# Performance work log

Hardware: AMD Instinct MI355X
Metric: run time of the kernel (lower is better)

## Reference

```python
import jax, jax.numpy as jnp
import numpy as np

B, S, M, D, H = 2, 2048, 512, 1024, 16
HD = D // H      # head dim 64
KVC = D // 16    # MLA kv compression dim 64
QC = D // 32     # MLA q compression dim 32
RD = HD          # retrieval (qk) head dim 64
LOOKBACK = 8     # cross_window
EPS = 1e-6


def rmsnorm(x, w):
    return x * jax.lax.rsqrt(jnp.mean(x * x, axis=-1, keepdims=True) + EPS) * w


def setup_inputs():
    key = jax.random.key(0)
    ks = jax.random.split(key, 20)
    g = lambda i, shape: jax.random.normal(ks[i], shape, jnp.float32) * 0.02
    return {
        "x": jax.random.normal(ks[0], (B, S, D), jnp.float32),
        "memory": jax.random.normal(ks[1], (B, M, D), jnp.float32),
        "seg_ids": jnp.sort(jax.random.randint(ks[2], (B, S), 0, M), axis=-1),
        "norm1_w": jnp.ones((D,), jnp.float32),
        "W_dq": g(3, (D, QC)),
        "W_uq": g(4, (QC, H * RD)),
        "W_dkv": g(5, (D, KVC)),
        "W_uk": g(6, (KVC, H * RD)),
        "W_uv": g(7, (KVC, H * HD)),
        "W_o_self": g(8, (H * HD, D)),
        "norm2_w": jnp.ones((D,), jnp.float32),
        "W_q_c": g(9, (D, D)),
        "W_k_c": g(10, (D, D)),
        "W_v_c": g(11, (D, D)),
        "W_o_c": g(12, (D, D)),
        "norm3_w": jnp.ones((D,), jnp.float32),
        "W_gate": g(13, (D, 4 * D)),
        "W_up": g(14, (D, 4 * D)),
        "W_down": g(15, (4 * D, D)),
    }


def reference(x, memory, seg_ids, norm1_w, W_dq, W_uq, W_dkv, W_uk, W_uv,
              W_o_self, norm2_w, W_q_c, W_k_c, W_v_c, W_o_c, norm3_w,
              W_gate, W_up, W_down):
    # ---- MLA causal self-attention (low-rank compressed q/kv) ----
    h = rmsnorm(x, norm1_w)
    q = ((h @ W_dq) @ W_uq).reshape(B, S, H, RD)
    c_kv = h @ W_dkv                                  # [B,S,KVC]
    k = (c_kv @ W_uk).reshape(B, S, H, RD)
    v = (c_kv @ W_uv).reshape(B, S, H, HD)
    scores = jnp.einsum('bihd,bjhd->bhij', q, k) / np.float32(np.sqrt(RD))
    causal = jnp.tril(jnp.ones((S, S), bool))
    scores = jnp.where(causal, scores, -jnp.inf)
    attn = jax.nn.softmax(scores, axis=-1)
    o = jnp.einsum('bhij,bjhd->bihd', attn, v).reshape(B, S, H * HD)
    x = x + o @ W_o_self
    # ---- segment sliding-window cross-attention ----
    h = rmsnorm(x, norm2_w)
    qc = (h @ W_q_c).reshape(B, S, H, HD)
    kc = (memory @ W_k_c).reshape(B, M, H, HD)
    vc = (memory @ W_v_c).reshape(B, M, H, HD)
    sc = jnp.einsum('bihd,bjhd->bhij', qc, kc) / np.float32(np.sqrt(HD))
    kv_pos = jnp.arange(M)
    seg = seg_ids[:, :, None]                          # [B,S,1]
    allowed = (kv_pos[None, None, :] <= seg) & (kv_pos[None, None, :] >= seg - LOOKBACK)
    sc = jnp.where(allowed[:, None, :, :], sc, -jnp.inf)
    ac = jax.nn.softmax(sc, axis=-1)
    oc = jnp.einsum('bhij,bjhd->bihd', ac, vc).reshape(B, S, D)
    x = x + oc @ W_o_c
    # ---- SwiGLU FFN ----
    h = rmsnorm(x, norm3_w)
    x = x + (jax.nn.silu(h @ W_gate) * (h @ W_up)) @ W_down
    return x
```

## Files before the change

### kernel.cpp

```cpp
#include <hip/hip_runtime.h>
#include <stdint.h>

typedef unsigned short U16;
typedef __bf16 bf16x8 __attribute__((ext_vector_type(8)));
typedef unsigned short us8 __attribute__((ext_vector_type(8)));
typedef float f32x4 __attribute__((ext_vector_type(4)));

__device__ __forceinline__ U16 f2bf(float f) {
    unsigned u = __builtin_bit_cast(unsigned, f);
    unsigned r = (u + 0x7fff + ((u >> 16) & 1)) >> 16;
    return (U16)r;
}
__device__ __forceinline__ float bf2f(U16 v) {
    return __builtin_bit_cast(float, (unsigned)v << 16);
}
__device__ __forceinline__ bf16x8 ld8(const U16* p) { return __builtin_bit_cast(bf16x8, *(const us8*)p); }

__device__ __forceinline__ void async16(const U16* g, U16* l) {
    auto* gp = (const __attribute__((address_space(1))) U16*)g;
    auto* lp = (__attribute__((address_space(3))) U16*)(uintptr_t)(uint32_t)(uintptr_t)l;
    __builtin_amdgcn_global_load_lds(gp, lp, 16, 0, 0);
}

struct WEnt { const float* src; U16* dst; int K, N, Kpad, Npad, koff, noff, tiles; };
struct WTable { WEnt e[13]; };

__global__ __launch_bounds__(256) void wtrans_all(WTable t) {
    int bx = blockIdx.x, ei = 0;
    while (bx >= t.e[ei].tiles) { bx -= t.e[ei].tiles; ei++; }
    const WEnt E = t.e[ei];
    const int ntn = E.Npad >> 5;
    const int n0 = (bx % ntn) * 32, k0 = (bx / ntn) * 32;
    __shared__ float tile[32][33];
    const int tx = threadIdx.x & 31, ty = threadIdx.x >> 5;
#pragma unroll
    for (int i = 0; i < 4; i++) {
        int kk = k0 + ty + i * 8, n = n0 + tx;
        int k = kk - E.koff;
        float v = (k >= 0 && k < E.K && n < E.N) ? E.src[(size_t)k * E.N + n] : 0.f;
        tile[ty + i * 8][tx] = v;
    }
    __syncthreads();
#pragma unroll
    for (int i = 0; i < 4; i++) {
        int n = n0 + ty + i * 8, kk = k0 + tx;
        E.dst[(size_t)(E.noff + n) * E.Kpad + kk] = f2bf(tile[tx][ty + i * 8]);
    }
}

__global__ __launch_bounds__(256) void f2bf_k(const float* __restrict__ in, U16* __restrict__ out, int n) {
    int i = (blockIdx.x * 256 + threadIdx.x) * 4;
    if (i < n) {
        float4 v = *(const float4*)(in + i);
        out[i + 0] = f2bf(v.x); out[i + 1] = f2bf(v.y);
        out[i + 2] = f2bf(v.z); out[i + 3] = f2bf(v.w);
    }
}

__global__ __launch_bounds__(256) void rmsnorm_k(const float* __restrict__ x, const float* __restrict__ w,
                                                 U16* __restrict__ h) {
    const int row = blockIdx.x, tid = threadIdx.x;
    const float4 v = *(const float4*)(x + (size_t)row * 1024 + tid * 4);
    float ss = v.x * v.x + v.y * v.y + v.z * v.z + v.w * v.w;
#pragma unroll
    for (int o = 32; o > 0; o >>= 1) ss += __shfl_xor(ss, o);
    __shared__ float red[4];
    if ((tid & 63) == 0) red[tid >> 6] = ss;
    __syncthreads();
    float tot = red[0] + red[1] + red[2] + red[3];
    float sc = rsqrtf(tot * (1.0f / 1024.0f) + 1e-6f);
    const float4 wv = *(const float4*)(w + tid * 4);
    U16* hp = h + (size_t)row * 1024 + tid * 4;
    hp[0] = f2bf(v.x * sc * wv.x); hp[1] = f2bf(v.y * sc * wv.y);
    hp[2] = f2bf(v.z * sc * wv.z); hp[3] = f2bf(v.w * sc * wv.w);
}

template <int EPI>
__global__ __launch_bounds__(256) void gemm2(const U16* __restrict__ A, const U16* __restrict__ Bt,
                                             void* __restrict__ Cout, const float* __restrict__ resid,
                                             int M, int N, int K, int lda, int ldc) {
    __shared__ __align__(16) U16 As[2][128 * 32];
    __shared__ __align__(16) U16 Bs[2][128 * 32];
    const int tid = threadIdx.x;
    const int m0 = blockIdx.y * 128, n0 = blockIdx.x * 128;
    const int wave = tid >> 6, lane = tid & 63, l16 = lane & 15, quad = lane >> 4;
    const int wm = (wave >> 1) * 64, wn = (wave & 1) * 64;
    const int sr = lane >> 2, sc = (lane & 3) * 8;
    const U16* gA = A + (size_t)(m0 + wave * 32 + sr) * lda + sc;
    const U16* gB = Bt + (size_t)(n0 + wave * 32 + sr) * K + sc;
    f32x4 acc[4][4] = {};
    for (int kt = 0; kt < K; kt += 64) {
        __syncthreads();
#pragma unroll
        for (int p = 0; p < 2; p++) {
            const int o = kt + p * 32;
            async16(gA + o, &As[p][(wave * 32) * 32]);
            async16(gA + (size_t)16 * lda + o, &As[p][(wave * 32 + 16) * 32]);
            async16(gB + o, &Bs[p][(wave * 32) * 32]);
            async16(gB + (size_t)16 * K + o, &Bs[p][(wave * 32 + 16) * 32]);
        }
        __syncthreads();
#pragma unroll
        for (int p = 0; p < 2; p++) {
            bf16x8 af[4], bfr[4];
#pragma unroll
            for (int i = 0; i < 4; i++) {
                af[i]  = ld8(&As[p][(wm + i * 16 + l16) * 32 + quad * 8]);
                bfr[i] = ld8(&Bs[p][(wn + i * 16 + l16) * 32 + quad * 8]);
            }
#pragma unroll
            for (int mi = 0; mi < 4; mi++)
#pragma unroll
                for (int ni = 0; ni < 4; ni++)
                    acc[mi][ni] = __builtin_amdgcn_mfma_f32_16x16x32_bf16(af[mi], bfr[ni], acc[mi][ni], 0, 0, 0);
        }
    }
#pragma unroll
    for (int mi = 0; mi < 4; mi++) {
#pragma unroll
        for (int r = 0; r < 4; r++) {
            int m = m0 + wm + mi * 16 + quad * 4 + r;
#pragma unroll
            for (int ni = 0; ni < 4; ni++) {
                int n = n0 + wn + ni * 16 + l16;
                float val = acc[mi][ni][r];
                if (EPI == 0) ((U16*)Cout)[(size_t)m * ldc + n] = f2bf(val);
                else if (EPI == 1) ((float*)Cout)[(size_t)m * ldc + n] = resid[(size_t)m * ldc + n] + val;
                else ((U16*)Cout)[(size_t)n * ldc + m] = f2bf(val);
            }
        }
    }
}

template <int EPI>
__global__ __launch_bounds__(256) void gemm_m64(const U16* __restrict__ A, const U16* __restrict__ Bt,
                                                void* __restrict__ Cout, const float* __restrict__ resid,
                                                int M, int N, int K, int lda, int ldb, int ldc) {
    __shared__ __align__(16) U16 As[4][64 * 32];
    __shared__ __align__(16) U16 Bs[4][128 * 32];
    const int tid = threadIdx.x;
    const int m0 = blockIdx.y * 64, n0 = blockIdx.x * 128;
    const int k0 = blockIdx.z * K;
    const int wave = tid >> 6, lane = tid & 63, l16 = lane & 15, quad = lane >> 4;
    const int wm = (wave >> 1) * 32, wn = (wave & 1) * 64;
    const int sr = lane >> 2, sc = (lane & 3) * 8;
    const U16* gA = A + (size_t)(m0 + wave * 16 + sr) * lda + sc + k0;
    const U16* gB = Bt + (size_t)(n0 + wave * 32 + sr) * ldb + sc + k0;
    f32x4 acc[2][4] = {};
    for (int kt = 0; kt < K; kt += 128) {
        __syncthreads();
#pragma unroll
        for (int p = 0; p < 4; p++) {
            const int o = kt + p * 32;
            async16(gA + o, &As[p][(wave * 16) * 32]);
            async16(gB + o, &Bs[p][(wave * 32) * 32]);
            async16(gB + (size_t)16 * ldb + o, &Bs[p][(wave * 32 + 16) * 32]);
        }
        __syncthreads();
#pragma unroll
        for (int p = 0; p < 4; p++) {
            bf16x8 af[2], bfr[4];
#pragma unroll
            for (int i = 0; i < 2; i++)
                af[i] = ld8(&As[p][(wm + i * 16 + l16) * 32 + quad * 8]);
#pragma unroll
            for (int i = 0; i < 4; i++)
                bfr[i] = ld8(&Bs[p][(wn + i * 16 + l16) * 32 + quad * 8]);
#pragma unroll
            for (int mi = 0; mi < 2; mi++)
#pragma unroll
                for (int ni = 0; ni < 4; ni++)
                    acc[mi][ni] = __builtin_amdgcn_mfma_f32_16x16x32_bf16(af[mi], bfr[ni], acc[mi][ni], 0, 0, 0);
        }
    }
#pragma unroll
    for (int mi = 0; mi < 2; mi++) {
#pragma unroll
        for (int r = 0; r < 4; r++) {
            int m = m0 + wm + mi * 16 + quad * 4 + r;
#pragma unroll
            for (int ni = 0; ni < 4; ni++) {
                int n = n0 + wn + ni * 16 + l16;
                float val = acc[mi][ni][r];
                if (EPI == 0) ((U16*)Cout)[(size_t)m * ldc + n] = f2bf(val);
                else if (EPI == 1) ((float*)Cout)[(size_t)m * ldc + n] = resid[(size_t)m * ldc + n] + val;
                else if (EPI == 3) atomicAdd(&((float*)Cout)[(size_t)m * ldc + n], val);
            }
        }
    }
}

__global__ __launch_bounds__(256) void ffn1_fused(const U16* __restrict__ A, const U16* __restrict__ Wgu,
                                                  U16* __restrict__ Cout) {
    __shared__ __align__(16) U16 As[2][128 * 32];
    __shared__ __align__(16) U16 Gs[2][64 * 32];
    __shared__ __align__(16) U16 Us[2][64 * 32];
    const int tid = threadIdx.x;
    const int m0 = blockIdx.y * 128, n0 = blockIdx.x * 64;
    const int wave = tid >> 6, lane = tid & 63, l16 = lane & 15, quad = lane >> 4;
    const int wm = (wave >> 1) * 64, wn = (wave & 1) * 32;
    const int sr = lane >> 2, sc = (lane & 3) * 8;
    const U16* gA = A + (size_t)(m0 + wave * 32 + sr) * 1024 + sc;
    const U16* gG = Wgu + (size_t)(n0 + wave * 16 + sr) * 1024 + sc;
    const U16* gU = gG + (size_t)4096 * 1024;
    f32x4 ag[4][2] = {}, au[4][2] = {};
    for (int kt = 0; kt < 1024; kt += 64) {
        __syncthreads();
#pragma unroll
        for (int p = 0; p < 2; p++) {
            const int o = kt + p * 32;
            async16(gA + o, &As[p][(wave * 32) * 32]);
            async16(gA + 16 * 1024 + o, &As[p][(wave * 32 + 16) * 32]);
            async16(gG + o, &Gs[p][(wave * 16) * 32]);
            async16(gU + o, &Us[p][(wave * 16) * 32]);
        }
        __syncthreads();
#pragma unroll
        for (int p = 0; p < 2; p++) {
            bf16x8 af[4], bg[2], bu[2];
#pragma unroll
            for (int i = 0; i < 4; i++)
                af[i] = ld8(&As[p][(wm + i * 16 + l16) * 32 + quad * 8]);
#pragma unroll
            for (int i = 0; i < 2; i++) {
                bg[i] = ld8(&Gs[p][(wn + i * 16 + l16) * 32 + quad * 8]);
                bu[i] = ld8(&Us[p][(wn + i * 16 + l16) * 32 + quad * 8]);
            }
#pragma unroll
            for (int mi = 0; mi < 4; mi++)
#pragma unroll
                for (int ni = 0; ni < 2; ni++) {
                    ag[mi][ni] = __builtin_amdgcn_mfma_f32_16x16x32_bf16(af[mi], bg[ni], ag[mi][ni], 0, 0, 0);
                    au[mi][ni] = __builtin_amdgcn_mfma_f32_16x16x32_bf16(af[mi], bu[ni], au[mi][ni], 0, 0, 0);
                }
        }
    }
#pragma unroll
    for (int mi = 0; mi < 4; mi++) {
#pragma unroll
        for (int r = 0; r < 4; r++) {
            int m = m0 + wm + mi * 16 + quad * 4 + r;
#pragma unroll
            for (int ni = 0; ni < 2; ni++) {
                int n = n0 + wn + ni * 16 + l16;
                float g = ag[mi][ni][r], u = au[mi][ni][r];
                float act = g / (1.f + __expf(-g)) * u;
                Cout[(size_t)m * 4096 + n] = f2bf(act);
            }
        }
    }
}

__global__ __launch_bounds__(256) void flash_self3(const U16* __restrict__ QK, const U16* __restrict__ Vt,
                                                   U16* __restrict__ Og) {
    __shared__ __align__(16) U16 Ps[4 * 1280];
    __shared__ float Ored[4 * 2080];
    __shared__ float Lred[128];
    const int wave = threadIdx.x >> 6, lane = threadIdx.x & 63;
    const int l16 = lane & 15, quad = lane >> 4;
    const int bx = blockIdx.x;
    const int t = 63 - (bx >> 5);
    const int bh = bx & 31, b = bh >> 4, h = bh & 15;
    const int q0 = t * 32;
    const size_t rowQ0 = (size_t)(b * 2048 + q0 + l16) * 2048 + h * 64;
    const size_t rowQ1 = rowQ0 + 16 * 2048;
    bf16x8 aq[2][2];
    aq[0][0] = ld8(QK + rowQ0 + quad * 8);  aq[0][1] = ld8(QK + rowQ0 + 32 + quad * 8);
    aq[1][0] = ld8(QK + rowQ1 + quad * 8);  aq[1][1] = ld8(QK + rowQ1 + 32 + quad * 8);
    const U16* Kbase = QK + (size_t)(b * 2048) * 2048 + 1024 + h * 64;
    const U16* Vbase = Vt + (size_t)(h * 64) * 4096 + b * 2048;
    f32x4 o[2][4] = {};
    float ls[2][4] = {};
    U16* Pw = &Ps[wave * 1280];
    const int prd = l16 * 40 + ((quad ^ (l16 >> 2)) << 3);
    const int jend = q0 + 32;
    for (int j0 = wave * 32; j0 < jend; j0 += 128) {
        const U16* kp = Kbase + (size_t)j0 * 2048;
        bf16x8 b00 = ld8(kp + (size_t)l16 * 2048 + quad * 8);
        bf16x8 b01 = ld8(kp + (size_t)l16 * 2048 + 32 + quad * 8);
        bf16x8 b10 = ld8(kp + (size_t)(16 + l16) * 2048 + quad * 8);
        bf16x8 b11 = ld8(kp + (size_t)(16 + l16) * 2048 + 32 + quad * 8);
        bf16x8 v0 = ld8(Vbase + (size_t)(0  + l16) * 4096 + j0 + quad * 8);
        bf16x8 v1 = ld8(Vbase + (size_t)(16 + l16) * 4096 + j0 + quad * 8);
        bf16x8 v2 = ld8(Vbase + (size_t)(32 + l16) * 4096 + j0 + quad * 8);
        bf16x8 v3 = ld8(Vbase + (size_t)(48 + l16) * 4096 + j0 + quad * 8);
        f32x4 s[2][2] = {};
#pragma unroll
        for (int g = 0; g < 2; g++) {
            s[g][0] = __builtin_amdgcn_mfma_f32_16x16x32_bf16(aq[g][0], b00, s[g][0], 0, 0, 0);
            s[g][0] = __builtin_amdgcn_mfma_f32_16x16x32_bf16(aq[g][1], b01, s[g][0], 0, 0, 0);
            s[g][1] = __builtin_amdgcn_mfma_f32_16x16x32_bf16(aq[g][0], b10, s[g][1], 0, 0, 0);
            s[g][1] = __builtin_amdgcn_mfma_f32_16x16x32_bf16(aq[g][1], b11, s[g][1], 0, 0, 0);
        }
        float p0[2][4], p1[2][4];
        if (j0 + 32 >= jend) {
#pragma unroll
            for (int g = 0; g < 2; g++)
#pragma unroll
                for (int r = 0; r < 4; r++) {
                    int qg = q0 + g * 16 + quad * 4 + r;
                    p0[g][r] = (j0 + l16 <= qg) ? __expf(fminf(s[g][0][r] * 0.125f, 30.f)) : 0.f;
                    p1[g][r] = (j0 + 16 + l16 <= qg) ? __expf(fminf(s[g][1][r] * 0.125f, 30.f)) : 0.f;
                }
        } else {
#pragma unroll
            for (int g = 0; g < 2; g++)
#pragma unroll
                for (int r = 0; r < 4; r++) {
                    p0[g][r] = __expf(fminf(s[g][0][r] * 0.125f, 30.f));
                    p1[g][r] = __expf(fminf(s[g][1][r] * 0.125f, 30.f));
                }
        }
#pragma unroll
        for (int g = 0; g < 2; g++)
#pragma unroll
            for (int r = 0; r < 4; r++) {
                ls[g][r] += p0[g][r] + p1[g][r];
                int row = quad * 4 + r;
                Pw[g * 640 + row * 40 + ((((l16 >> 3) + 0) ^ quad) << 3) + (l16 & 7)] = f2bf(p0[g][r]);
                Pw[g * 640 + row * 40 + ((((l16 >> 3) + 2) ^ quad) << 3) + (l16 & 7)] = f2bf(p1[g][r]);
            }
#pragma unroll
        for (int g = 0; g < 2; g++) {
            bf16x8 ap = ld8(&Pw[g * 640 + prd]);
            o[g][0] = __builtin_amdgcn_mfma_f32_16x16x32_bf16(ap, v0, o[g][0], 0, 0, 0);
            o[g][1] = __builtin_amdgcn_mfma_f32_16x16x32_bf16(ap, v1, o[g][1], 0, 0, 0);
            o[g][2] = __builtin_amdgcn_mfma_f32_16x16x32_bf16(ap, v2, o[g][2], 0, 0, 0);
            o[g][3] = __builtin_amdgcn_mfma_f32_16x16x32_bf16(ap, v3, o[g][3], 0, 0, 0);
        }
    }
    float* Or = &Ored[wave * 2080];
#pragma unroll
    for (int g = 0; g < 2; g++) {
#pragma unroll
        for (int dg = 0; dg < 4; dg++)
#pragma unroll
            for (int r = 0; r < 4; r++)
                Or[(g * 16 + quad * 4 + r) * 65 + dg * 16 + l16] = o[g][dg][r];
#pragma unroll
        for (int r = 0; r < 4; r++) {
            float v = ls[g][r];
            v += __shfl_xor(v, 1); v += __shfl_xor(v, 2);
            v += __shfl_xor(v, 4); v += __shfl_xor(v, 8);
            if (l16 == 0) Lred[wave * 32 + g * 16 + quad * 4 + r] = v;
        }
    }
    __syncthreads();
    const int q = threadIdx.x >> 3, d0 = (threadIdx.x & 7) * 8;
    float l = Lred[q] + Lred[32 + q] + Lred[64 + q] + Lred[96 + q];
    float inv = 1.0f / l;
    us8 outv;
#pragma unroll
    for (int i = 0; i < 8; i++) {
        int idx = q * 65 + d0 + i;
        float s = Ored[idx] + Ored[2080 + idx] + Ored[4160 + idx] + Ored[6240 + idx];
        outv[i] = f2bf(s * inv);
    }
    *(us8*)(Og + (size_t)(b * 2048 + q0 + q) * 1024 + h * 64 + d0) = outv;
}

__global__ __launch_bounds__(256) void cross_attn(const U16* __restrict__ qc, const U16* __restrict__ kvc,
                                                  const int* __restrict__ seg_ids, U16* __restrict__ oc) {
    const int tok = blockIdx.x;
    const int b = tok >> 11;
    const int w = threadIdx.x >> 6, lane = threadIdx.x & 63;
    const int h = blockIdx.y * 4 + w;
    const int seg = seg_ids[tok];
    const size_t qoff = (size_t)tok * 1024 + h * 64 + lane;
    float q = bf2f(qc[qoff]);
    float s[9];
#pragma unroll
    for (int jj = 0; jj < 9; jj++) {
        int j = seg - 8 + jj;
        float sc = -INFINITY;
        if (j >= 0) {
            float kv = bf2f(kvc[((size_t)(b * 512) + j) * 2048 + h * 64 + lane]);
            sc = q * kv;
            sc += __shfl_xor(sc, 1); sc += __shfl_xor(sc, 2); sc += __shfl_xor(sc, 4);
            sc += __shfl_xor(sc, 8); sc += __shfl_xor(sc, 16); sc += __shfl_xor(sc, 32);
            sc *= 0.125f;
        }
        s[jj] = sc;
    }
    float m = s[0];
#pragma unroll
    for (int jj = 1; jj < 9; jj++) m = fmaxf(m, s[jj]);
    float l = 0.f, o = 0.f;
#pragma unroll
    for (int jj = 0; jj < 9; jj++) {
        int j = seg - 8 + jj;
        if (j >= 0) {
            float p = __expf(s[jj] - m);
            l += p;
            o += p * bf2f(kvc[((size_t)(b * 512) + j) * 2048 + 1024 + h * 64 + lane]);
        }
    }
    oc[qoff] = f2bf(o / l);
}

extern "C" void kernel_launch(void* const* d_in, const int* in_sizes, int n_in,
                              void* d_out, int out_size, void* d_ws, size_t ws_size,
                              hipStream_t stream) {
    const float* x      = (const float*)d_in[0];
    const float* memory = (const float*)d_in[1];
    const int*   seg    = (const int*)d_in[2];
    const float* n1w    = (const float*)d_in[3];
    const float* W_dq   = (const float*)d_in[4];
    const float* W_uq   = (const float*)d_in[5];
    const float* W_dkv  = (const float*)d_in[6];
    const float* W_uk   = (const float*)d_in[7];
    const float* W_uv   = (const float*)d_in[8];
    const float* W_os   = (const float*)d_in[9];
    const float* n2w    = (const float*)d_in[10];
    const float* W_qc   = (const float*)d_in[11];
    const float* W_kc   = (const float*)d_in[12];
    const float* W_vc   = (const float*)d_in[13];
    const float* W_oc   = (const float*)d_in[14];
    const float* n3w    = (const float*)d_in[15];
    const float* W_gate = (const float*)d_in[16];
    const float* W_up   = (const float*)d_in[17];
    const float* W_down = (const float*)d_in[18];
    (void)in_sizes; (void)n_in; (void)out_size; (void)ws_size;

    char* ws = (char*)d_ws;
    size_t off = 0;
    auto alloc = [&](size_t bytes) -> void* {
        void* p = ws + off;
        off += (bytes + 255) & ~(size_t)255;
        return p;
    };
    const size_t MB = 1024 * 1024;
    U16* hbuf     = (U16*)alloc(8 * MB);
    float* x1     = (float*)alloc(16 * MB);
    float* x2     = (float*)alloc(16 * MB);
    float* cq32   = (float*)alloc(2 * MB);
    U16* Wt_dqkv  = (U16*)alloc(128 * 1024 * 2);
    U16* Wt_uqk   = (U16*)alloc(2048 * 128 * 2);
    U16* Wt_uv    = (U16*)alloc(1024 * 128 * 2);
    U16* Wt_os    = (U16*)alloc(1024 * 1024 * 2);
    U16* Wt_qc    = (U16*)alloc(1024 * 1024 * 2);
    U16* Wt_kvc   = (U16*)alloc((size_t)2048 * 1024 * 2);
    U16* Wt_oc    = (U16*)alloc(1024 * 1024 * 2);
    U16* Wt_gu    = (U16*)alloc((size_t)8192 * 1024 * 2);
    U16* Wt_down  = (U16*)alloc((size_t)1024 * 4096 * 2);
    U16* mem_bf   = (U16*)alloc(1024 * 1024 * 2);
    char* arena   = ws + off;
    U16* cq  = (U16*)(arena);
    U16* qkb = (U16*)(arena + 1 * MB);
    U16* vt  = (U16*)(arena + 17 * MB);
    U16* ob  = (U16*)(arena + 25 * MB);
    U16* qcb  = (U16*)(arena);
    U16* kvcb = (U16*)(arena + 8 * MB);
    U16* ocb  = (U16*)(arena + 12 * MB);
    U16* gact = (U16*)(arena);

    WTable T;
    int i = 0;
    auto ent = [&](const float* s, U16* d, int K, int N, int Kpad, int Npad, int koff, int noff) {
        T.e[i++] = WEnt{s, d, K, N, Kpad, Npad, koff, noff, (Kpad >> 5) * (Npad >> 5)};
    };
    ent(W_dq,   Wt_dqkv, 1024, 32,   1024, 32,   0,  0);
    ent(W_dkv,  Wt_dqkv, 1024, 64,   1024, 96,   0,  32);
    ent(W_uq,   Wt_uqk,  32,   1024, 128,  1024, 0,  0);
    ent(W_uk,   Wt_uqk,  64,   1024, 128,  1024, 32, 1024);
    ent(W_uv,   Wt_uv,   64,   1024, 128,  1024, 32, 0);
    ent(W_os,   Wt_os,   1024, 1024, 1024, 1024, 0,  0);
    ent(W_qc,   Wt_qc,   1024, 1024, 1024, 1024, 0,  0);
    ent(W_kc,   Wt_kvc,  1024, 1024, 1024, 1024, 0,  0);
    ent(W_vc,   Wt_kvc,  1024, 1024, 1024, 1024, 0,  1024);
    ent(W_oc,   Wt_oc,   1024, 1024, 1024, 1024, 0,  0);
    ent(W_gate, Wt_gu,   1024, 4096, 1024, 4096, 0,  0);
    ent(W_up,   Wt_gu,   1024, 4096, 1024, 4096, 0,  4096);
    ent(W_down, Wt_down, 4096, 1024, 4096, 1024, 0,  0);
    int total_tiles = 0;
    for (int j = 0; j < 13; j++) total_tiles += T.e[j].tiles;
    wtrans_all<<<total_tiles, 256, 0, stream>>>(T);
    f2bf_k<<<1024, 256, 0, stream>>>(memory, mem_bf, 1024 * 1024);
    hipMemsetAsync(cq32, 0, (size_t)4096 * 128 * 4, stream);

    rmsnorm_k<<<4096, 256, 0, stream>>>(x, n1w, hbuf);
    gemm_m64<3><<<dim3(1, 64, 4), 256, 0, stream>>>(hbuf, Wt_dqkv, cq32, nullptr, 4096, 128, 256, 1024, 1024, 128);
    f2bf_k<<<512, 256, 0, stream>>>(cq32, cq, 4096 * 128);
    gemm2<0><<<dim3(16, 32), 256, 0, stream>>>(cq, Wt_uqk, qkb, nullptr, 4096, 2048, 128, 128, 2048);
    gemm2<2><<<dim3(8, 32),  256, 0, stream>>>(cq, Wt_uv,  vt,  nullptr, 4096, 1024, 128, 128, 4096);
    flash_self3<<<2048, 256, 0, stream>>>(qkb, vt, ob);
    gemm_m64<1><<<dim3(8, 64), 256, 0, stream>>>(ob, Wt_os, x1, x, 4096, 1024, 1024, 1024, 1024, 1024);

    rmsnorm_k<<<4096, 256, 0, stream>>>(x1, n2w, hbuf);
    gemm_m64<0><<<dim3(8, 64),  256, 0, stream>>>(hbuf,   Wt_qc,  qcb,  nullptr, 4096, 1024, 1024, 1024, 1024, 1024);
    gemm_m64<0><<<dim3(16, 16), 256, 0, stream>>>(mem_bf, Wt_kvc, kvcb, nullptr, 1024, 2048, 1024, 1024, 1024, 2048);
    cross_attn<<<dim3(4096, 4), 256, 0, stream>>>(qcb, kvcb, seg, ocb);
    gemm_m64<1><<<dim3(8, 64),  256, 0, stream>>>(ocb,    Wt_oc,  x2,   x1,      4096, 1024, 1024, 1024, 1024, 1024);

    rmsnorm_k<<<4096, 256, 0, stream>>>(x2, n3w, hbuf);
    ffn1_fused<<<dim3(64, 32), 256, 0, stream>>>(hbuf, Wt_gu, gact);
    gemm_m64<1><<<dim3(8, 64), 256, 0, stream>>>(gact, Wt_down, (float*)d_out, x2, 4096, 1024, 4096, 4096, 4096, 1024);
}
```

Baseline: 553.5 us.

## Split-K down-projection with atomic adds, LDS-staged transpose epilogue, faster bf16 rounding

The FFN down-projection now runs on the 128x128 gemm2 tile with the K=4096 reduction split in two along grid z. Each half atomically adds into a zero-initialised output, and the first half also adds the residual. The transposed-V epilogue of gemm2 now stages results through LDS and writes 16-byte coalesced rows instead of scattered 2-byte stores. The softmax P conversion also uses a cheaper round-half-up bf16 conversion. These add an output memset, a second LDS buffer and fp32 atomics, which make the output summation order nondeterministic.

```diff
diff --git a/kernel.cpp b/kernel.cpp
--- a/kernel.cpp
+++ b/kernel.cpp
@@ -10,6 +10,9 @@
     unsigned u = __builtin_bit_cast(unsigned, f);
     unsigned r = (u + 0x7fff + ((u >> 16) & 1)) >> 16;
     return (U16)r;
+}
+__device__ __forceinline__ U16 f2bf_fast(float f) {
+    return (U16)((__builtin_bit_cast(unsigned, f) + 0x8000u) >> 16);
 }
 __device__ __forceinline__ float bf2f(U16 v) {
     return __builtin_bit_cast(float, (unsigned)v << 16);
@@ -78,16 +81,17 @@
 template <int EPI>
 __global__ __launch_bounds__(256) void gemm2(const U16* __restrict__ A, const U16* __restrict__ Bt,
                                              void* __restrict__ Cout, const float* __restrict__ resid,
-                                             int M, int N, int K, int lda, int ldc) {
+                                             int M, int N, int K, int lda, int ldb, int ldc) {
     __shared__ __align__(16) U16 As[2][128 * 32];
     __shared__ __align__(16) U16 Bs[2][128 * 32];
     const int tid = threadIdx.x;
     const int m0 = blockIdx.y * 128, n0 = blockIdx.x * 128;
+    const int k0 = blockIdx.z * K;
     const int wave = tid >> 6, lane = tid & 63, l16 = lane & 15, quad = lane >> 4;
     const int wm = (wave >> 1) * 64, wn = (wave & 1) * 64;
     const int sr = lane >> 2, sc = (lane & 3) * 8;
-    const U16* gA = A + (size_t)(m0 + wave * 32 + sr) * lda + sc;
-    const U16* gB = Bt + (size_t)(n0 + wave * 32 + sr) * K + sc;
+    const U16* gA = A + (size_t)(m0 + wave * 32 + sr) * lda + sc + k0;
+    const U16* gB = Bt + (size_t)(n0 + wave * 32 + sr) * ldb + sc + k0;
     f32x4 acc[4][4] = {};
     for (int kt = 0; kt < K; kt += 64) {
         __syncthreads();
@@ -97,7 +101,7 @@
             async16(gA + o, &As[p][(wave * 32) * 32]);
             async16(gA + (size_t)16 * lda + o, &As[p][(wave * 32 + 16) * 32]);
             async16(gB + o, &Bs[p][(wave * 32) * 32]);
-            async16(gB + (size_t)16 * K + o, &Bs[p][(wave * 32 + 16) * 32]);
+            async16(gB + (size_t)16 * ldb + o, &Bs[p][(wave * 32 + 16) * 32]);
         }
         __syncthreads();
 #pragma unroll
@@ -115,18 +119,38 @@
                     acc[mi][ni] = __builtin_amdgcn_mfma_f32_16x16x32_bf16(af[mi], bfr[ni], acc[mi][ni], 0, 0, 0);
         }
     }
-#pragma unroll
-    for (int mi = 0; mi < 4; mi++) {
-#pragma unroll
-        for (int r = 0; r < 4; r++) {
-            int m = m0 + wm + mi * 16 + quad * 4 + r;
-#pragma unroll
-            for (int ni = 0; ni < 4; ni++) {
-                int n = n0 + wn + ni * 16 + l16;
-                float val = acc[mi][ni][r];
-                if (EPI == 0) ((U16*)Cout)[(size_t)m * ldc + n] = f2bf(val);
-                else if (EPI == 1) ((float*)Cout)[(size_t)m * ldc + n] = resid[(size_t)m * ldc + n] + val;
-                else ((U16*)Cout)[(size_t)n * ldc + m] = f2bf(val);
+    if constexpr (EPI == 2) {
+        __shared__ __align__(16) U16 Ts[4][64 * 80];
+        U16* T = Ts[wave];
+#pragma unroll
+        for (int mi = 0; mi < 4; mi++)
+#pragma unroll
+            for (int ni = 0; ni < 4; ni++)
+#pragma unroll
+                for (int r = 0; r < 4; r++)
+                    T[(ni * 16 + l16) * 80 + mi * 16 + quad * 4 + r] = f2bf(acc[mi][ni][r]);
+#pragma unroll
+        for (int c = 0; c < 8; c++) {
+            int nloc = (lane >> 3) + 8 * c, mloc = (lane & 7) * 8;
+            us8 v = *(const us8*)&T[nloc * 80 + mloc];
+            *(us8*)&((U16*)Cout)[(size_t)(n0 + wn + nloc) * ldc + (m0 + wm + mloc)] = v;
+        }
+    } else {
+#pragma unroll
+        for (int mi = 0; mi < 4; mi++) {
+#pragma unroll
+            for (int r = 0; r < 4; r++) {
+                int m = m0 + wm + mi * 16 + quad * 4 + r;
+#pragma unroll
+                for (int ni = 0; ni < 4; ni++) {
+                    int n = n0 + wn + ni * 16 + l16;
+                    float val = acc[mi][ni][r];
+                    if (EPI == 0) ((U16*)Cout)[(size_t)m * ldc + n] = f2bf(val);
+                    else if (EPI == 4) {
+                        if (blockIdx.z == 0) val += resid[(size_t)m * ldc + n];
+                        atomicAdd(&((float*)Cout)[(size_t)m * ldc + n], val);
+                    }
+                }
             }
         }
     }
@@ -317,8 +341,8 @@
             for (int r = 0; r < 4; r++) {
                 ls[g][r] += p0[g][r] + p1[g][r];
                 int row = quad * 4 + r;
-                Pw[g * 640 + row * 40 + ((((l16 >> 3) + 0) ^ quad) << 3) + (l16 & 7)] = f2bf(p0[g][r]);
-                Pw[g * 640 + row * 40 + ((((l16 >> 3) + 2) ^ quad) << 3) + (l16 & 7)] = f2bf(p1[g][r]);
+                Pw[g * 640 + row * 40 + ((((l16 >> 3) + 0) ^ quad) << 3) + (l16 & 7)] = f2bf_fast(p0[g][r]);
+                Pw[g * 640 + row * 40 + ((((l16 >> 3) + 2) ^ quad) << 3) + (l16 & 7)] = f2bf_fast(p1[g][r]);
             }
 #pragma unroll
         for (int g = 0; g < 2; g++) {
@@ -477,12 +501,13 @@
     wtrans_all<<<total_tiles, 256, 0, stream>>>(T);
     f2bf_k<<<1024, 256, 0, stream>>>(memory, mem_bf, 1024 * 1024);
     hipMemsetAsync(cq32, 0, (size_t)4096 * 128 * 4, stream);
+    hipMemsetAsync(d_out, 0, (size_t)4096 * 1024 * 4, stream);
 
     rmsnorm_k<<<4096, 256, 0, stream>>>(x, n1w, hbuf);
     gemm_m64<3><<<dim3(1, 64, 4), 256, 0, stream>>>(hbuf, Wt_dqkv, cq32, nullptr, 4096, 128, 256, 1024, 1024, 128);
     f2bf_k<<<512, 256, 0, stream>>>(cq32, cq, 4096 * 128);
-    gemm2<0><<<dim3(16, 32), 256, 0, stream>>>(cq, Wt_uqk, qkb, nullptr, 4096, 2048, 128, 128, 2048);
-    gemm2<2><<<dim3(8, 32),  256, 0, stream>>>(cq, Wt_uv,  vt,  nullptr, 4096, 1024, 128, 128, 4096);
+    gemm2<0><<<dim3(16, 32), 256, 0, stream>>>(cq, Wt_uqk, qkb, nullptr, 4096, 2048, 128, 128, 128, 2048);
+    gemm2<2><<<dim3(8, 32),  256, 0, stream>>>(cq, Wt_uv,  vt,  nullptr, 4096, 1024, 128, 128, 128, 4096);
     flash_self3<<<2048, 256, 0, stream>>>(qkb, vt, ob);
     gemm_m64<1><<<dim3(8, 64), 256, 0, stream>>>(ob, Wt_os, x1, x, 4096, 1024, 1024, 1024, 1024, 1024);
 
@@ -494,5 +519,5 @@
 
     rmsnorm_k<<<4096, 256, 0, stream>>>(x2, n3w, hbuf);
     ffn1_fused<<<dim3(64, 32), 256, 0, stream>>>(hbuf, Wt_gu, gact);
-    gemm_m64<1><<<dim3(8, 64), 256, 0, stream>>>(gact, Wt_down, (float*)d_out, x2, 4096, 1024, 4096, 4096, 4096, 1024);
-}
+    gemm2<4><<<dim3(8, 32, 2), 256, 0, stream>>>(gact, Wt_down, (float*)d_out, x2, 4096, 1024, 2048, 4096, 4096, 1024);
+}
```

Measured after the change: 580.1 us. +4.8%, slower.
